# Kernel tuning notes

Hardware: AMD Instinct MI355X
Metric: run time of the kernel (lower is better)

Reference implementation:

```python
import jax, jax.numpy as jnp
import numpy as np

NUM_LABELS = 10000
HIDDEN = 1024
B = 256
K = 4096


def setup_inputs() -> dict:
    key = jax.random.key(0)
    k1, k2, k3, k4, k5, k6 = jax.random.split(key, 6)
    embeddings = jax.random.normal(k1, (B, HIDDEN), dtype=jnp.float32)
    W1 = jax.random.normal(k2, (NUM_LABELS, 8, HIDDEN), dtype=jnp.float32) * 0.02
    b1 = jax.random.normal(k3, (NUM_LABELS, 8), dtype=jnp.float32) * 0.02
    W2 = jax.random.normal(k4, (NUM_LABELS, 1, 8), dtype=jnp.float32) * 0.02
    b2 = jax.random.normal(k5, (NUM_LABELS, 1), dtype=jnp.float32) * 0.02
    task_ids = jax.random.randint(k6, (K,), 0, NUM_LABELS, dtype=jnp.int64)
    return {"embeddings": embeddings, "W1": W1, "b1": b1, "W2": W2, "b2": b2, "task_ids": task_ids}


def reference(embeddings, W1, b1, W2, b2, task_ids):
    # Gather the selected heads (irregular access over the 10k-head tables).
    w1 = W1[task_ids]      # [K, 8, H]
    bb1 = b1[task_ids]     # [K, 8]
    w2 = W2[task_ids]      # [K, 1, 8]
    bb2 = b2[task_ids]     # [K, 1]
    # Batched tiny MLP: Linear(H,8) -> ReLU -> Linear(8,1), grouped over K heads.
    h = jax.nn.relu(jnp.einsum('bh,koh->kbo', embeddings, w1) + bb1[:, None, :])  # [K, B, 8]
    out = jnp.einsum('kbo,kio->kbi', h, w2) + bb2[:, None, :]                     # [K, B, 1]
    # torch: cat([head(emb).squeeze(-1) for ...], dim=-1) -> flat [K*B], task-major.
    return out[..., 0].reshape(-1)
```

## Files before the change

### kernel.cpp

```cpp
#include <hip/hip_runtime.h>

#define HID 1024
#define BATCH 256
#define KTASK 4096
#define TPB 8
#define NCOL 64
#define KC 32
#define NSTEPS (HID / KC)
#define STRIDE 80

typedef __bf16 bf16x8 __attribute__((ext_vector_type(8)));
typedef __bf16 bf16x4 __attribute__((ext_vector_type(4)));
typedef float f32x4 __attribute__((ext_vector_type(4)));

static __device__ __forceinline__ bf16x8 cvt8(const float4& a, const float4& b) {
    bf16x8 r;
    r[0] = (__bf16)a.x; r[1] = (__bf16)a.y; r[2] = (__bf16)a.z; r[3] = (__bf16)a.w;
    r[4] = (__bf16)b.x; r[5] = (__bf16)b.y; r[6] = (__bf16)b.z; r[7] = (__bf16)b.w;
    return r;
}

__global__ __launch_bounds__(256, 4)
void cvt_emb_kernel(const float* __restrict__ emb, __bf16* __restrict__ dst) {
    int i = (blockIdx.x * 256 + threadIdx.x) * 4;
    float4 v = *(const float4*)(emb + i);
    bf16x4 r;
    r[0] = (__bf16)v.x; r[1] = (__bf16)v.y; r[2] = (__bf16)v.z; r[3] = (__bf16)v.w;
    *(bf16x4*)(dst + i) = r;
}

__global__ __launch_bounds__(256, 4)
void mtc_kernel(const __bf16* __restrict__ embb, const float* __restrict__ W1,
                const float* __restrict__ b1, const float* __restrict__ W2,
                const float* __restrict__ b2, const int* __restrict__ tids,
                float* __restrict__ out)
{
    __shared__ __align__(16) char wbuf[2][NCOL * STRIDE];

    const int t = threadIdx.x;
    const int lane = t & 63;
    const int w = t >> 6;
    const int sw = (blockIdx.x & 7) * 128 + (blockIdx.x >> 3);
    const int tg = sw >> 1;
    const int mh = sw & 1;

    const int srow = t >> 2;
    const int sq   = t & 3;
    const int stask = tids[tg * TPB + (srow >> 3)];
    const float* sgp = W1 + (size_t)stask * (8 * HID) + (size_t)(srow & 7) * HID + sq * 8;
    char* const swr0 = &wbuf[0][0] + srow * STRIDE + sq * 16;
    char* const swr1 = swr0 + NCOL * STRIDE;

    const __bf16* agp = embb + (size_t)(mh * 128 + w * 32 + (lane & 15)) * HID + (lane >> 4) * 8;
    const int boff = (lane & 15) * STRIDE + (lane >> 4) * 16;
    const char* const rb0 = &wbuf[0][0];
    const char* const rb1 = &wbuf[1][0];

    f32x4 acc[2][4];
    const f32x4 zero = {0.f, 0.f, 0.f, 0.f};
#pragma unroll
    for (int i = 0; i < 2; ++i)
#pragma unroll
        for (int j = 0; j < 4; ++j) acc[i][j] = zero;

    float4 wa0 = *(const float4*)(sgp);
    float4 wa1 = *(const float4*)(sgp + 4);
    bf16x8 acur0 = *(const bf16x8*)(agp);
    bf16x8 acur1 = *(const bf16x8*)(agp + 16 * HID);
    *(bf16x8*)swr0 = cvt8(wa0, wa1);
    float4 wb0 = *(const float4*)(sgp + KC);
    float4 wb1 = *(const float4*)(sgp + KC + 4);
    __syncthreads();

    for (int i = 0; i < 15; ++i) {
        const int s = 2 * i;
        {
            wa0 = *(const float4*)(sgp + (s + 2) * KC);
            wa1 = *(const float4*)(sgp + (s + 2) * KC + 4);
            bf16x8 an0 = *(const bf16x8*)(agp + (s + 1) * KC);
            bf16x8 an1 = *(const bf16x8*)(agp + (s + 1) * KC + 16 * HID);
#pragma unroll
            for (int nt = 0; nt < 4; ++nt) {
                bf16x8 bf = *(const bf16x8*)(rb0 + nt * (16 * STRIDE) + boff);
                acc[0][nt] = __builtin_amdgcn_mfma_f32_16x16x32_bf16(acur0, bf, acc[0][nt], 0, 0, 0);
                acc[1][nt] = __builtin_amdgcn_mfma_f32_16x16x32_bf16(acur1, bf, acc[1][nt], 0, 0, 0);
            }
            *(bf16x8*)swr1 = cvt8(wb0, wb1);
            acur0 = an0; acur1 = an1;
            __syncthreads();
        }
        {
            wb0 = *(const float4*)(sgp + (s + 3) * KC);
            wb1 = *(const float4*)(sgp + (s + 3) * KC + 4);
            bf16x8 an0 = *(const bf16x8*)(agp + (s + 2) * KC);
            bf16x8 an1 = *(const bf16x8*)(agp + (s + 2) * KC + 16 * HID);
#pragma unroll
            for (int nt = 0; nt < 4; ++nt) {
                bf16x8 bf = *(const bf16x8*)(rb1 + nt * (16 * STRIDE) + boff);
                acc[0][nt] = __builtin_amdgcn_mfma_f32_16x16x32_bf16(acur0, bf, acc[0][nt], 0, 0, 0);
                acc[1][nt] = __builtin_amdgcn_mfma_f32_16x16x32_bf16(acur1, bf, acc[1][nt], 0, 0, 0);
            }
            *(bf16x8*)swr0 = cvt8(wa0, wa1);
            acur0 = an0; acur1 = an1;
            __syncthreads();
        }
    }
    {
        bf16x8 an0 = *(const bf16x8*)(agp + 31 * KC);
        bf16x8 an1 = *(const bf16x8*)(agp + 31 * KC + 16 * HID);
#pragma unroll
        for (int nt = 0; nt < 4; ++nt) {
            bf16x8 bf = *(const bf16x8*)(rb0 + nt * (16 * STRIDE) + boff);
            acc[0][nt] = __builtin_amdgcn_mfma_f32_16x16x32_bf16(acur0, bf, acc[0][nt], 0, 0, 0);
            acc[1][nt] = __builtin_amdgcn_mfma_f32_16x16x32_bf16(acur1, bf, acc[1][nt], 0, 0, 0);
        }
        *(bf16x8*)swr1 = cvt8(wb0, wb1);
        acur0 = an0; acur1 = an1;
        __syncthreads();
    }
    {
#pragma unroll
        for (int nt = 0; nt < 4; ++nt) {
            bf16x8 bf = *(const bf16x8*)(rb1 + nt * (16 * STRIDE) + boff);
            acc[0][nt] = __builtin_amdgcn_mfma_f32_16x16x32_bf16(acur0, bf, acc[0][nt], 0, 0, 0);
            acc[1][nt] = __builtin_amdgcn_mfma_f32_16x16x32_bf16(acur1, bf, acc[1][nt], 0, 0, 0);
        }
    }

    const int col = lane & 15;
    const int rgrp = lane >> 4;
    const int o = col & 7;
#pragma unroll
    for (int nt = 0; nt < 4; ++nt) {
        const int tl = nt * 2 + (col >> 3);
        const int task = tids[tg * TPB + tl];
        const float bb1 = b1[task * 8 + o];
        const float ww2 = W2[task * 8 + o];
#pragma unroll
        for (int bt = 0; bt < 2; ++bt) {
            float v[4];
#pragma unroll
            for (int r = 0; r < 4; ++r) {
                float x = acc[bt][nt][r] + bb1;
                x = x > 0.f ? x : 0.f;
                v[r] = x * ww2;
            }
#pragma unroll
            for (int m = 1; m <= 4; m <<= 1) {
#pragma unroll
                for (int r = 0; r < 4; ++r) v[r] += __shfl_xor(v[r], m, 64);
            }
            if ((lane & 7) == 0) {
                const float bb2 = b2[task];
                const int brow = mh * 128 + w * 32 + bt * 16 + rgrp * 4;
                float4 o4 = make_float4(v[0] + bb2, v[1] + bb2, v[2] + bb2, v[3] + bb2);
                *(float4*)(out + (size_t)(tg * TPB + tl) * BATCH + brow) = o4;
            }
        }
    }
}

extern "C" void kernel_launch(void* const* d_in, const int* in_sizes, int n_in,
                              void* d_out, int out_size, void* d_ws, size_t ws_size,
                              hipStream_t stream) {
    const float* emb = (const float*)d_in[0];
    const float* W1  = (const float*)d_in[1];
    const float* b1  = (const float*)d_in[2];
    const float* W2  = (const float*)d_in[3];
    const float* b2  = (const float*)d_in[4];
    const int*   tid = (const int*)d_in[5];
    float* outp = (float*)d_out;
    __bf16* embb = (__bf16*)d_ws;

    cvt_emb_kernel<<<dim3(BATCH * HID / (256 * 4)), dim3(256), 0, stream>>>(emb, embb);
    mtc_kernel<<<dim3(1024), dim3(256), 0, stream>>>(embb, W1, b1, W2, b2, tid, outp);
}
```

Measured before the change: 54.04 us.

## Retile grouped MLP so each block covers full batch for four tasks

Each block now handles 4 tasks (32 weight columns) across all 256 batch rows, instead of 8 tasks across half the batch. The gathered W1 rows are loaded and converted once rather than twice, which halves fp32 W1 traffic per task. In exchange each block reads the full bf16 embedding matrix and keeps more accumulators and A fragments per wave (4x2 tiles). The grid stays at 1024 blocks, and the XCD-aware block swizzle is dropped.

```diff
diff --git a/kernel.cpp b/kernel.cpp
--- a/kernel.cpp
+++ b/kernel.cpp
@@ -3,8 +3,8 @@
 #define HID 1024
 #define BATCH 256
 #define KTASK 4096
-#define TPB 8
-#define NCOL 64
+#define TPB 4
+#define NCOL (TPB * 8)
 #define KC 32
 #define NSTEPS (HID / KC)
 #define STRIDE 80
@@ -13,10 +13,9 @@
 typedef __bf16 bf16x4 __attribute__((ext_vector_type(4)));
 typedef float f32x4 __attribute__((ext_vector_type(4)));
 
-static __device__ __forceinline__ bf16x8 cvt8(const float4& a, const float4& b) {
-    bf16x8 r;
+static __device__ __forceinline__ bf16x4 cvt4(const float4& a) {
+    bf16x4 r;
     r[0] = (__bf16)a.x; r[1] = (__bf16)a.y; r[2] = (__bf16)a.z; r[3] = (__bf16)a.w;
-    r[4] = (__bf16)b.x; r[5] = (__bf16)b.y; r[6] = (__bf16)b.z; r[7] = (__bf16)b.w;
     return r;
 }
 
@@ -24,9 +23,7 @@
 void cvt_emb_kernel(const float* __restrict__ emb, __bf16* __restrict__ dst) {
     int i = (blockIdx.x * 256 + threadIdx.x) * 4;
     float4 v = *(const float4*)(emb + i);
-    bf16x4 r;
-    r[0] = (__bf16)v.x; r[1] = (__bf16)v.y; r[2] = (__bf16)v.z; r[3] = (__bf16)v.w;
-    *(bf16x4*)(dst + i) = r;
+    *(bf16x4*)(dst + i) = cvt4(v);
 }
 
 __global__ __launch_bounds__(256, 4)
@@ -40,90 +37,98 @@
     const int t = threadIdx.x;
     const int lane = t & 63;
     const int w = t >> 6;
-    const int sw = (blockIdx.x & 7) * 128 + (blockIdx.x >> 3);
-    const int tg = sw >> 1;
-    const int mh = sw & 1;
+    const int blk = blockIdx.x;
 
-    const int srow = t >> 2;
-    const int sq   = t & 3;
-    const int stask = tids[tg * TPB + (srow >> 3)];
-    const float* sgp = W1 + (size_t)stask * (8 * HID) + (size_t)(srow & 7) * HID + sq * 8;
-    char* const swr0 = &wbuf[0][0] + srow * STRIDE + sq * 16;
+    const int srow = t >> 3;
+    const int sq   = t & 7;
+    const int stask = tids[blk * TPB + (srow >> 3)];
+    const float* sgp = W1 + (size_t)stask * (8 * HID) + (size_t)(srow & 7) * HID + sq * 4;
+    char* const swr0 = &wbuf[0][0] + srow * STRIDE + sq * 8;
     char* const swr1 = swr0 + NCOL * STRIDE;
 
-    const __bf16* agp = embb + (size_t)(mh * 128 + w * 32 + (lane & 15)) * HID + (lane >> 4) * 8;
+    const __bf16* agp = embb + (size_t)(w * 64 + (lane & 15)) * HID + (lane >> 4) * 8;
     const int boff = (lane & 15) * STRIDE + (lane >> 4) * 16;
     const char* const rb0 = &wbuf[0][0];
     const char* const rb1 = &wbuf[1][0];
 
-    f32x4 acc[2][4];
+    f32x4 acc[4][2];
     const f32x4 zero = {0.f, 0.f, 0.f, 0.f};
 #pragma unroll
-    for (int i = 0; i < 2; ++i)
+    for (int i = 0; i < 4; ++i)
 #pragma unroll
-        for (int j = 0; j < 4; ++j) acc[i][j] = zero;
+        for (int j = 0; j < 2; ++j) acc[i][j] = zero;
 
-    float4 wa0 = *(const float4*)(sgp);
-    float4 wa1 = *(const float4*)(sgp + 4);
-    bf16x8 acur0 = *(const bf16x8*)(agp);
-    bf16x8 acur1 = *(const bf16x8*)(agp + 16 * HID);
-    *(bf16x8*)swr0 = cvt8(wa0, wa1);
-    float4 wb0 = *(const float4*)(sgp + KC);
-    float4 wb1 = *(const float4*)(sgp + KC + 4);
+    float4 wa = *(const float4*)(sgp);
+    bf16x8 acur[4];
+#pragma unroll
+    for (int bt = 0; bt < 4; ++bt) acur[bt] = *(const bf16x8*)(agp + (size_t)bt * (16 * HID));
+    *(bf16x4*)swr0 = cvt4(wa);
+    float4 wb = *(const float4*)(sgp + KC);
     __syncthreads();
 
     for (int i = 0; i < 15; ++i) {
         const int s = 2 * i;
         {
-            wa0 = *(const float4*)(sgp + (s + 2) * KC);
-            wa1 = *(const float4*)(sgp + (s + 2) * KC + 4);
-            bf16x8 an0 = *(const bf16x8*)(agp + (s + 1) * KC);
-            bf16x8 an1 = *(const bf16x8*)(agp + (s + 1) * KC + 16 * HID);
+            wa = *(const float4*)(sgp + (s + 2) * KC);
+            bf16x8 an[4];
 #pragma unroll
-            for (int nt = 0; nt < 4; ++nt) {
+            for (int bt = 0; bt < 4; ++bt)
+                an[bt] = *(const bf16x8*)(agp + (s + 1) * KC + (size_t)bt * (16 * HID));
+#pragma unroll
+            for (int nt = 0; nt < 2; ++nt) {
                 bf16x8 bf = *(const bf16x8*)(rb0 + nt * (16 * STRIDE) + boff);
-                acc[0][nt] = __builtin_amdgcn_mfma_f32_16x16x32_bf16(acur0, bf, acc[0][nt], 0, 0, 0);
-                acc[1][nt] = __builtin_amdgcn_mfma_f32_16x16x32_bf16(acur1, bf, acc[1][nt], 0, 0, 0);
+#pragma unroll
+                for (int bt = 0; bt < 4; ++bt)
+                    acc[bt][nt] = __builtin_amdgcn_mfma_f32_16x16x32_bf16(acur[bt], bf, acc[bt][nt], 0, 0, 0);
             }
-            *(bf16x8*)swr1 = cvt8(wb0, wb1);
-            acur0 = an0; acur1 = an1;
+            *(bf16x4*)swr1 = cvt4(wb);
+#pragma unroll
+            for (int bt = 0; bt < 4; ++bt) acur[bt] = an[bt];
             __syncthreads();
         }
         {
-            wb0 = *(const float4*)(sgp + (s + 3) * KC);
-            wb1 = *(const float4*)(sgp + (s + 3) * KC + 4);
-            bf16x8 an0 = *(const bf16x8*)(agp + (s + 2) * KC);
-            bf16x8 an1 = *(const bf16x8*)(agp + (s + 2) * KC + 16 * HID);
+            wb = *(const float4*)(sgp + (s + 3) * KC);
+            bf16x8 an[4];
 #pragma unroll
-            for (int nt = 0; nt < 4; ++nt) {
+            for (int bt = 0; bt < 4; ++bt)
+                an[bt] = *(const bf16x8*)(agp + (s + 2) * KC + (size_t)bt * (16 * HID));
+#pragma unroll
+            for (int nt = 0; nt < 2; ++nt) {
                 bf16x8 bf = *(const bf16x8*)(rb1 + nt * (16 * STRIDE) + boff);
-                acc[0][nt] = __builtin_amdgcn_mfma_f32_16x16x32_bf16(acur0, bf, acc[0][nt], 0, 0, 0);
-                acc[1][nt] = __builtin_amdgcn_mfma_f32_16x16x32_bf16(acur1, bf, acc[1][nt], 0, 0, 0);
+#pragma unroll
+                for (int bt = 0; bt < 4; ++bt)
+                    acc[bt][nt] = __builtin_amdgcn_mfma_f32_16x16x32_bf16(acur[bt], bf, acc[bt][nt], 0, 0, 0);
             }
-            *(bf16x8*)swr0 = cvt8(wa0, wa1);
-            acur0 = an0; acur1 = an1;
+            *(bf16x4*)swr0 = cvt4(wa);
+#pragma unroll
+            for (int bt = 0; bt < 4; ++bt) acur[bt] = an[bt];
             __syncthreads();
         }
     }
     {
-        bf16x8 an0 = *(const bf16x8*)(agp + 31 * KC);
-        bf16x8 an1 = *(const bf16x8*)(agp + 31 * KC + 16 * HID);
+        bf16x8 an[4];
 #pragma unroll
-        for (int nt = 0; nt < 4; ++nt) {
+        for (int bt = 0; bt < 4; ++bt)
+            an[bt] = *(const bf16x8*)(agp + 31 * KC + (size_t)bt * (16 * HID));
+#pragma unroll
+        for (int nt = 0; nt < 2; ++nt) {
             bf16x8 bf = *(const bf16x8*)(rb0 + nt * (16 * STRIDE) + boff);
-            acc[0][nt] = __builtin_amdgcn_mfma_f32_16x16x32_bf16(acur0, bf, acc[0][nt], 0, 0, 0);
-            acc[1][nt] = __builtin_amdgcn_mfma_f32_16x16x32_bf16(acur1, bf, acc[1][nt], 0, 0, 0);
+#pragma unroll
+            for (int bt = 0; bt < 4; ++bt)
+                acc[bt][nt] = __builtin_amdgcn_mfma_f32_16x16x32_bf16(acur[bt], bf, acc[bt][nt], 0, 0, 0);
         }
-        *(bf16x8*)swr1 = cvt8(wb0, wb1);
-        acur0 = an0; acur1 = an1;
+        *(bf16x4*)swr1 = cvt4(wb);
+#pragma unroll
+        for (int bt = 0; bt < 4; ++bt) acur[bt] = an[bt];
         __syncthreads();
     }
     {
 #pragma unroll
-        for (int nt = 0; nt < 4; ++nt) {
+        for (int nt = 0; nt < 2; ++nt) {
             bf16x8 bf = *(const bf16x8*)(rb1 + nt * (16 * STRIDE) + boff);
-            acc[0][nt] = __builtin_amdgcn_mfma_f32_16x16x32_bf16(acur0, bf, acc[0][nt], 0, 0, 0);
-            acc[1][nt] = __builtin_amdgcn_mfma_f32_16x16x32_bf16(acur1, bf, acc[1][nt], 0, 0, 0);
+#pragma unroll
+            for (int bt = 0; bt < 4; ++bt)
+                acc[bt][nt] = __builtin_amdgcn_mfma_f32_16x16x32_bf16(acur[bt], bf, acc[bt][nt], 0, 0, 0);
         }
     }
 
@@ -131,13 +136,13 @@
     const int rgrp = lane >> 4;
     const int o = col & 7;
 #pragma unroll
-    for (int nt = 0; nt < 4; ++nt) {
+    for (int nt = 0; nt < 2; ++nt) {
         const int tl = nt * 2 + (col >> 3);
-        const int task = tids[tg * TPB + tl];
+        const int task = tids[blk * TPB + tl];
         const float bb1 = b1[task * 8 + o];
         const float ww2 = W2[task * 8 + o];
 #pragma unroll
-        for (int bt = 0; bt < 2; ++bt) {
+        for (int bt = 0; bt < 4; ++bt) {
             float v[4];
 #pragma unroll
             for (int r = 0; r < 4; ++r) {
@@ -152,9 +157,9 @@
             }
             if ((lane & 7) == 0) {
                 const float bb2 = b2[task];
-                const int brow = mh * 128 + w * 32 + bt * 16 + rgrp * 4;
+                const int brow = w * 64 + bt * 16 + rgrp * 4;
                 float4 o4 = make_float4(v[0] + bb2, v[1] + bb2, v[2] + bb2, v[3] + bb2);
-                *(float4*)(out + (size_t)(tg * TPB + tl) * BATCH + brow) = o4;
+                *(float4*)(out + (size_t)(blk * TPB + tl) * BATCH + brow) = o4;
             }
         }
     }
@@ -173,5 +178,5 @@
     __bf16* embb = (__bf16*)d_ws;
 
     cvt_emb_kernel<<<dim3(BATCH * HID / (256 * 4)), dim3(256), 0, stream>>>(emb, embb);
-    mtc_kernel<<<dim3(1024), dim3(256), 0, stream>>>(embb, W1, b1, W2, b2, tid, outp);
+    mtc_kernel<<<dim3(KTASK / TPB), dim3(256), 0, stream>>>(embb, W1, b1, W2, b2, tid, outp);
 }
```

Result: slower. 75.53 us (+39.8%).

## Cover full batch per block with 512 threads to halve W1 gather traffic

Applied to the files above, without the earlier changes.

Each block now processes all 256 batch rows for its 8 tasks with 8 waves, instead of splitting the batch across two blocks. Each gathered W1 tile is therefore loaded and converted once rather than twice, which halves global W1 reads. Each thread now stages 4 floats instead of 8 per step. The trade-offs are half as many blocks (512), larger blocks with a heavier barrier cost, and removal of the block-index swizzle that grouped blocks for L2 locality.

```diff
diff --git a/kernel.cpp b/kernel.cpp
--- a/kernel.cpp
+++ b/kernel.cpp
@@ -4,7 +4,7 @@
 #define BATCH 256
 #define KTASK 4096
 #define TPB 8
-#define NCOL 64
+#define NCOL (TPB * 8)
 #define KC 32
 #define NSTEPS (HID / KC)
 #define STRIDE 80
@@ -13,10 +13,9 @@
 typedef __bf16 bf16x4 __attribute__((ext_vector_type(4)));
 typedef float f32x4 __attribute__((ext_vector_type(4)));
 
-static __device__ __forceinline__ bf16x8 cvt8(const float4& a, const float4& b) {
-    bf16x8 r;
+static __device__ __forceinline__ bf16x4 cvt4(const float4& a) {
+    bf16x4 r;
     r[0] = (__bf16)a.x; r[1] = (__bf16)a.y; r[2] = (__bf16)a.z; r[3] = (__bf16)a.w;
-    r[4] = (__bf16)b.x; r[5] = (__bf16)b.y; r[6] = (__bf16)b.z; r[7] = (__bf16)b.w;
     return r;
 }
 
@@ -24,12 +23,10 @@
 void cvt_emb_kernel(const float* __restrict__ emb, __bf16* __restrict__ dst) {
     int i = (blockIdx.x * 256 + threadIdx.x) * 4;
     float4 v = *(const float4*)(emb + i);
-    bf16x4 r;
-    r[0] = (__bf16)v.x; r[1] = (__bf16)v.y; r[2] = (__bf16)v.z; r[3] = (__bf16)v.w;
-    *(bf16x4*)(dst + i) = r;
+    *(bf16x4*)(dst + i) = cvt4(v);
 }
 
-__global__ __launch_bounds__(256, 4)
+__global__ __launch_bounds__(512, 4)
 void mtc_kernel(const __bf16* __restrict__ embb, const float* __restrict__ W1,
                 const float* __restrict__ b1, const float* __restrict__ W2,
                 const float* __restrict__ b2, const int* __restrict__ tids,
@@ -40,18 +37,16 @@
     const int t = threadIdx.x;
     const int lane = t & 63;
     const int w = t >> 6;
-    const int sw = (blockIdx.x & 7) * 128 + (blockIdx.x >> 3);
-    const int tg = sw >> 1;
-    const int mh = sw & 1;
+    const int blk = blockIdx.x;
 
-    const int srow = t >> 2;
-    const int sq   = t & 3;
-    const int stask = tids[tg * TPB + (srow >> 3)];
-    const float* sgp = W1 + (size_t)stask * (8 * HID) + (size_t)(srow & 7) * HID + sq * 8;
-    char* const swr0 = &wbuf[0][0] + srow * STRIDE + sq * 16;
+    const int srow = t >> 3;
+    const int sq   = t & 7;
+    const int stask = tids[blk * TPB + (srow >> 3)];
+    const float* sgp = W1 + (size_t)stask * (8 * HID) + (size_t)(srow & 7) * HID + sq * 4;
+    char* const swr0 = &wbuf[0][0] + srow * STRIDE + sq * 8;
     char* const swr1 = swr0 + NCOL * STRIDE;
 
-    const __bf16* agp = embb + (size_t)(mh * 128 + w * 32 + (lane & 15)) * HID + (lane >> 4) * 8;
+    const __bf16* agp = embb + (size_t)(w * 32 + (lane & 15)) * HID + (lane >> 4) * 8;
     const int boff = (lane & 15) * STRIDE + (lane >> 4) * 16;
     const char* const rb0 = &wbuf[0][0];
     const char* const rb1 = &wbuf[1][0];
@@ -63,20 +58,17 @@
 #pragma unroll
         for (int j = 0; j < 4; ++j) acc[i][j] = zero;
 
-    float4 wa0 = *(const float4*)(sgp);
-    float4 wa1 = *(const float4*)(sgp + 4);
+    float4 wa = *(const float4*)(sgp);
     bf16x8 acur0 = *(const bf16x8*)(agp);
     bf16x8 acur1 = *(const bf16x8*)(agp + 16 * HID);
-    *(bf16x8*)swr0 = cvt8(wa0, wa1);
-    float4 wb0 = *(const float4*)(sgp + KC);
-    float4 wb1 = *(const float4*)(sgp + KC + 4);
+    *(bf16x4*)swr0 = cvt4(wa);
+    float4 wb = *(const float4*)(sgp + KC);
     __syncthreads();
 
     for (int i = 0; i < 15; ++i) {
         const int s = 2 * i;
         {
-            wa0 = *(const float4*)(sgp + (s + 2) * KC);
-            wa1 = *(const float4*)(sgp + (s + 2) * KC + 4);
+            wa = *(const float4*)(sgp + (s + 2) * KC);
             bf16x8 an0 = *(const bf16x8*)(agp + (s + 1) * KC);
             bf16x8 an1 = *(const bf16x8*)(agp + (s + 1) * KC + 16 * HID);
 #pragma unroll
@@ -85,13 +77,12 @@
                 acc[0][nt] = __builtin_amdgcn_mfma_f32_16x16x32_bf16(acur0, bf, acc[0][nt], 0, 0, 0);
                 acc[1][nt] = __builtin_amdgcn_mfma_f32_16x16x32_bf16(acur1, bf, acc[1][nt], 0, 0, 0);
             }
-            *(bf16x8*)swr1 = cvt8(wb0, wb1);
+            *(bf16x4*)swr1 = cvt4(wb);
             acur0 = an0; acur1 = an1;
             __syncthreads();
         }
         {
-            wb0 = *(const float4*)(sgp + (s + 3) * KC);
-            wb1 = *(const float4*)(sgp + (s + 3) * KC + 4);
+            wb = *(const float4*)(sgp + (s + 3) * KC);
             bf16x8 an0 = *(const bf16x8*)(agp + (s + 2) * KC);
             bf16x8 an1 = *(const bf16x8*)(agp + (s + 2) * KC + 16 * HID);
 #pragma unroll
@@ -100,7 +91,7 @@
                 acc[0][nt] = __builtin_amdgcn_mfma_f32_16x16x32_bf16(acur0, bf, acc[0][nt], 0, 0, 0);
                 acc[1][nt] = __builtin_amdgcn_mfma_f32_16x16x32_bf16(acur1, bf, acc[1][nt], 0, 0, 0);
             }
-            *(bf16x8*)swr0 = cvt8(wa0, wa1);
+            *(bf16x4*)swr0 = cvt4(wa);
             acur0 = an0; acur1 = an1;
             __syncthreads();
         }
@@ -114,7 +105,7 @@
             acc[0][nt] = __builtin_amdgcn_mfma_f32_16x16x32_bf16(acur0, bf, acc[0][nt], 0, 0, 0);
             acc[1][nt] = __builtin_amdgcn_mfma_f32_16x16x32_bf16(acur1, bf, acc[1][nt], 0, 0, 0);
         }
-        *(bf16x8*)swr1 = cvt8(wb0, wb1);
+        *(bf16x4*)swr1 = cvt4(wb);
         acur0 = an0; acur1 = an1;
         __syncthreads();
     }
@@ -133,7 +124,7 @@
 #pragma unroll
     for (int nt = 0; nt < 4; ++nt) {
         const int tl = nt * 2 + (col >> 3);
-        const int task = tids[tg * TPB + tl];
+        const int task = tids[blk * TPB + tl];
         const float bb1 = b1[task * 8 + o];
         const float ww2 = W2[task * 8 + o];
 #pragma unroll
@@ -152,9 +143,9 @@
             }
             if ((lane & 7) == 0) {
                 const float bb2 = b2[task];
-                const int brow = mh * 128 + w * 32 + bt * 16 + rgrp * 4;
+                const int brow = w * 32 + bt * 16 + rgrp * 4;
                 float4 o4 = make_float4(v[0] + bb2, v[1] + bb2, v[2] + bb2, v[3] + bb2);
-                *(float4*)(out + (size_t)(tg * TPB + tl) * BATCH + brow) = o4;
+                *(float4*)(out + (size_t)(blk * TPB + tl) * BATCH + brow) = o4;
             }
         }
     }
@@ -173,5 +164,5 @@
     __bf16* embb = (__bf16*)d_ws;
 
     cvt_emb_kernel<<<dim3(BATCH * HID / (256 * 4)), dim3(256), 0, stream>>>(emb, embb);
-    mtc_kernel<<<dim3(1024), dim3(256), 0, stream>>>(embb, W1, b1, W2, b2, tid, outp);
+    mtc_kernel<<<dim3(KTASK / TPB), dim3(512), 0, stream>>>(embb, W1, b1, W2, b2, tid, outp);
 }
```

Result: faster. 50.09 us (-7.3%).
